# Optimization experiments

Hardware: AMD Instinct MI355X
Metric: run time of the kernel (lower is better)

Reference implementation:

```python
import jax, jax.numpy as jnp
import numpy as np

ALPHA_MAX = 0.1


def setup_inputs() -> dict:
    key = jax.random.key(0)
    ks = jax.random.split(key, 9)
    B, M, L = 256, 3, 100000
    A, H = 4096, 512
    return {
        "x": jax.random.uniform(ks[0], (B, M, L), dtype=jnp.float32),  # log1p scores, non-negative
        "active_idx": jax.random.randint(ks[1], (A,), 0, L, dtype=jnp.int64 if jax.config.jax_enable_x64 else jnp.int32),
        "global_logits": jnp.log(jnp.full((M,), 1.0 / M, dtype=jnp.float32) + 1e-12),
        "delta_w": 0.01 * jax.random.normal(ks[2], (M, L), dtype=jnp.float32),
        "bias": 0.01 * jax.random.normal(ks[3], (L,), dtype=jnp.float32),
        "log_alpha": jnp.float32(-3.0),
        "hidden_w": jax.random.normal(ks[4], (H, M * A), dtype=jnp.float32) * (1.0 / np.sqrt(M * A)),
        "hidden_b": 0.01 * jax.random.normal(ks[5], (H,), dtype=jnp.float32),
        "delta_layer_w": jax.random.normal(ks[6], (A, H), dtype=jnp.float32) * (1.0 / np.sqrt(H)),
        "delta_layer_b": 0.01 * jax.random.normal(ks[7], (A,), dtype=jnp.float32),
    }


def reference(x, active_idx, global_logits, delta_w, bias, log_alpha,
              hidden_w, hidden_b, delta_layer_w, delta_layer_b):
    B = x.shape[0]
    # base logits: elementwise weighted sum over the 3 models, per-label weights
    w_eff = jax.nn.softmax(global_logits)[:, None] + delta_w          # (M, L)
    logits = jnp.einsum("bml,ml->bl", x, w_eff) + bias                # (B, L)
    # gather active labels -> 2-layer MLP (dropout is identity in eval)
    x_active = x[:, :, active_idx].reshape(B, -1)                     # (B, M*A)
    h = jax.nn.relu(x_active @ hidden_w.T + hidden_b)                 # (B, H)
    delta_active = h @ delta_layer_w.T + delta_layer_b                # (B, A)
    # scaled scatter-add back into full logits (duplicates accumulate)
    alpha = ALPHA_MAX * jax.nn.sigmoid(log_alpha)
    logits = logits.at[:, active_idx].add(alpha * delta_active)
    return logits
```

## Files before the change

kernel.cpp:

```cpp
#include <hip/hip_runtime.h>
#include <math.h>

#define B_ 256
#define M_ 3
#define L_ 100000
#define A_ 4096
#define H_ 512
#define MA_ (M_*A_)
#define K1_ MA_
#define NZ_ 16
#define KC1_ (K1_/NZ_)
#define BCHUNK_ 4

typedef __attribute__((ext_vector_type(8))) short bf16x8;
typedef __attribute__((ext_vector_type(8))) unsigned short u16x8;
typedef __attribute__((ext_vector_type(4))) float f32x4;

static __device__ __forceinline__ float4 ld4(const float* p) {
    return *reinterpret_cast<const float4*>(p);
}
static __device__ __forceinline__ void st4(float* p, float4 v) {
    *reinterpret_cast<float4*>(p) = v;
}
static __device__ __forceinline__ unsigned short f2bf(float f) {
    unsigned u = __float_as_uint(f);
    unsigned r = (u + 0x7FFFu + ((u >> 16) & 1u)) >> 16;
    return (unsigned short)r;
}
static __device__ __forceinline__ float getc(const float4& v, int c) {
    switch (c) { case 0: return v.x; case 1: return v.y; case 2: return v.z; default: return v.w; }
}

__global__ void init_head(int* __restrict__ head) {
    int i = blockIdx.x * blockDim.x + threadIdx.x;
    if (i < L_) head[i] = -1;
}

__global__ void build_chain(const int* __restrict__ idx, int* __restrict__ head,
                            int* __restrict__ next) {
    int a = blockIdx.x * blockDim.x + threadIdx.x;
    if (a < A_) next[a] = atomicExch(&head[idx[a]], a);
}

__global__ void f32_to_bf16(const float* __restrict__ in, unsigned short* __restrict__ out, int n8) {
    int i = blockIdx.x * blockDim.x + threadIdx.x;
    if (i >= n8) return;
    float4 v0 = ld4(in + (size_t)i * 8);
    float4 v1 = ld4(in + (size_t)i * 8 + 4);
    u16x8 o;
    o[0] = f2bf(v0.x); o[1] = f2bf(v0.y); o[2] = f2bf(v0.z); o[3] = f2bf(v0.w);
    o[4] = f2bf(v1.x); o[5] = f2bf(v1.y); o[6] = f2bf(v1.z); o[7] = f2bf(v1.w);
    *reinterpret_cast<u16x8*>(out + (size_t)i * 8) = o;
}

__global__ __launch_bounds__(256) void logits_gather(
    const float* __restrict__ x, const float* __restrict__ gl,
    const float* __restrict__ dw, const float* __restrict__ bias,
    const int* __restrict__ head, const int* __restrict__ next,
    float* __restrict__ logits, unsigned short* __restrict__ xa) {
    const int L4 = L_ / 4;
    int i = blockIdx.x * blockDim.x + threadIdx.x;
    if (i >= L4) return;
    int l = i * 4;
    int b0 = blockIdx.y * BCHUNK_;

    float g0 = gl[0], g1 = gl[1], g2 = gl[2];
    float mx = fmaxf(g0, fmaxf(g1, g2));
    float e0 = expf(g0 - mx), e1 = expf(g1 - mx), e2 = expf(g2 - mx);
    float inv = 1.0f / (e0 + e1 + e2);
    float s0 = e0 * inv, s1 = e1 * inv, s2 = e2 * inv;

    float4 d0 = ld4(dw + l);
    float4 d1 = ld4(dw + L_ + l);
    float4 d2 = ld4(dw + 2 * L_ + l);
    float4 bb = ld4(bias + l);
    float4 w0 = make_float4(s0 + d0.x, s0 + d0.y, s0 + d0.z, s0 + d0.w);
    float4 w1 = make_float4(s1 + d1.x, s1 + d1.y, s1 + d1.z, s1 + d1.w);
    float4 w2 = make_float4(s2 + d2.x, s2 + d2.y, s2 + d2.z, s2 + d2.w);

    float4 X[BCHUNK_][3];
    #pragma unroll
    for (int c = 0; c < BCHUNK_; ++c) {
        const float* xb = x + (size_t)(b0 + c) * M_ * L_ + l;
        X[c][0] = ld4(xb);
        X[c][1] = ld4(xb + L_);
        X[c][2] = ld4(xb + 2 * L_);
    }
    #pragma unroll
    for (int c = 0; c < BCHUNK_; ++c) {
        float4 o;
        o.x = X[c][0].x * w0.x + X[c][1].x * w1.x + X[c][2].x * w2.x + bb.x;
        o.y = X[c][0].y * w0.y + X[c][1].y * w1.y + X[c][2].y * w2.y + bb.y;
        o.z = X[c][0].z * w0.z + X[c][1].z * w1.z + X[c][2].z * w2.z + bb.z;
        o.w = X[c][0].w * w0.w + X[c][1].w * w1.w + X[c][2].w * w2.w + bb.w;
        st4(logits + (size_t)(b0 + c) * L_ + l, o);
    }

    #pragma unroll
    for (int c = 0; c < 4; ++c) {
        int a = head[l + c];
        while (a >= 0) {
            #pragma unroll
            for (int b = 0; b < BCHUNK_; ++b) {
                unsigned short* xab = xa + (size_t)(b0 + b) * MA_;
                xab[a]            = f2bf(getc(X[b][0], c));
                xab[A_ + a]       = f2bf(getc(X[b][1], c));
                xab[2 * A_ + a]   = f2bf(getc(X[b][2], c));
            }
            a = next[a];
        }
    }
}

__global__ __launch_bounds__(256) void gemm1_mfma(
    const unsigned short* __restrict__ Xa, const unsigned short* __restrict__ W,
    float* __restrict__ part) {
    int tid = threadIdx.x;
    int wave = tid >> 6, lane = tid & 63;
    int row0 = blockIdx.x * 64 + (wave >> 1) * 32;
    int col0 = blockIdx.y * 64 + (wave & 1) * 32;
    int k0 = blockIdx.z * KC1_;
    int lr = lane & 15;
    int lk = (lane >> 4) * 8;
    const unsigned short* pa0 = Xa + (size_t)(row0 + lr) * K1_ + k0 + lk;
    const unsigned short* pa1 = pa0 + (size_t)16 * K1_;
    const unsigned short* pb0 = W + (size_t)(col0 + lr) * K1_ + k0 + lk;
    const unsigned short* pb1 = pb0 + (size_t)16 * K1_;
    f32x4 acc00 = {0.f,0.f,0.f,0.f}, acc01 = {0.f,0.f,0.f,0.f};
    f32x4 acc10 = {0.f,0.f,0.f,0.f}, acc11 = {0.f,0.f,0.f,0.f};
    #pragma unroll 4
    for (int k = 0; k < KC1_; k += 32) {
        bf16x8 a0 = *reinterpret_cast<const bf16x8*>(pa0 + k);
        bf16x8 a1 = *reinterpret_cast<const bf16x8*>(pa1 + k);
        bf16x8 b0 = *reinterpret_cast<const bf16x8*>(pb0 + k);
        bf16x8 b1 = *reinterpret_cast<const bf16x8*>(pb1 + k);
        acc00 = __builtin_amdgcn_mfma_f32_16x16x32_bf16(a0, b0, acc00, 0, 0, 0);
        acc01 = __builtin_amdgcn_mfma_f32_16x16x32_bf16(a0, b1, acc01, 0, 0, 0);
        acc10 = __builtin_amdgcn_mfma_f32_16x16x32_bf16(a1, b0, acc10, 0, 0, 0);
        acc11 = __builtin_amdgcn_mfma_f32_16x16x32_bf16(a1, b1, acc11, 0, 0, 0);
    }
    float* base = part + (size_t)blockIdx.z * B_ * H_;
    #pragma unroll
    for (int j = 0; j < 4; ++j) {
        int r = (lane >> 4) * 4 + j;
        base[(size_t)(row0 + r) * H_ + col0 + lr]           = acc00[j];
        base[(size_t)(row0 + r) * H_ + col0 + 16 + lr]      = acc01[j];
        base[(size_t)(row0 + 16 + r) * H_ + col0 + lr]      = acc10[j];
        base[(size_t)(row0 + 16 + r) * H_ + col0 + 16 + lr] = acc11[j];
    }
}

__global__ void reduce_relu(const float* __restrict__ part,
                            const float* __restrict__ hb,
                            unsigned short* __restrict__ h) {
    int t = blockIdx.x * blockDim.x + threadIdx.x;
    if (t >= B_ * H_) return;
    int n = t & (H_ - 1);
    float s = hb[n];
    #pragma unroll
    for (int z = 0; z < NZ_; ++z) s += part[(size_t)z * B_ * H_ + t];
    h[t] = f2bf(fmaxf(s, 0.0f));
}

__global__ __launch_bounds__(256) void gemm2_mfma(
    const unsigned short* __restrict__ Hm, const unsigned short* __restrict__ W2,
    const float* __restrict__ b2, const float* __restrict__ la,
    float* __restrict__ da) {
    int tid = threadIdx.x;
    int wave = tid >> 6, lane = tid & 63;
    int row0 = blockIdx.x * 64 + (wave >> 1) * 32;
    int col0 = blockIdx.y * 64 + (wave & 1) * 32;
    int lr = lane & 15;
    int lk = (lane >> 4) * 8;
    const unsigned short* pa0 = Hm + (size_t)(row0 + lr) * H_ + lk;
    const unsigned short* pa1 = pa0 + (size_t)16 * H_;
    const unsigned short* pb0 = W2 + (size_t)(col0 + lr) * H_ + lk;
    const unsigned short* pb1 = pb0 + (size_t)16 * H_;
    f32x4 acc00 = {0.f,0.f,0.f,0.f}, acc01 = {0.f,0.f,0.f,0.f};
    f32x4 acc10 = {0.f,0.f,0.f,0.f}, acc11 = {0.f,0.f,0.f,0.f};
    #pragma unroll 4
    for (int k = 0; k < H_; k += 32) {
        bf16x8 a0 = *reinterpret_cast<const bf16x8*>(pa0 + k);
        bf16x8 a1 = *reinterpret_cast<const bf16x8*>(pa1 + k);
        bf16x8 b0 = *reinterpret_cast<const bf16x8*>(pb0 + k);
        bf16x8 b1 = *reinterpret_cast<const bf16x8*>(pb1 + k);
        acc00 = __builtin_amdgcn_mfma_f32_16x16x32_bf16(a0, b0, acc00, 0, 0, 0);
        acc01 = __builtin_amdgcn_mfma_f32_16x16x32_bf16(a0, b1, acc01, 0, 0, 0);
        acc10 = __builtin_amdgcn_mfma_f32_16x16x32_bf16(a1, b0, acc10, 0, 0, 0);
        acc11 = __builtin_amdgcn_mfma_f32_16x16x32_bf16(a1, b1, acc11, 0, 0, 0);
    }
    float alpha = 0.1f / (1.0f + expf(-la[0]));
    #pragma unroll
    for (int j = 0; j < 4; ++j) {
        int r = (lane >> 4) * 4 + j;
        int c0 = col0 + lr, c1 = col0 + 16 + lr;
        da[(size_t)(row0 + r) * A_ + c0]      = alpha * (acc00[j] + b2[c0]);
        da[(size_t)(row0 + r) * A_ + c1]      = alpha * (acc01[j] + b2[c1]);
        da[(size_t)(row0 + 16 + r) * A_ + c0] = alpha * (acc10[j] + b2[c0]);
        da[(size_t)(row0 + 16 + r) * A_ + c1] = alpha * (acc11[j] + b2[c1]);
    }
}

__global__ void scatter_add(const float* __restrict__ da, const int* __restrict__ idx,
                            const int* __restrict__ head, const int* __restrict__ next,
                            float* __restrict__ logits) {
    int t = blockIdx.x * blockDim.x + threadIdx.x;
    if (t >= B_ * A_) return;
    int a = t & (A_ - 1);
    int b = t >> 12;
    int l = idx[a];
    if (head[l] != a) return;
    float s = 0.0f;
    for (int aa = a; aa >= 0; aa = next[aa]) s += da[(size_t)b * A_ + aa];
    logits[(size_t)b * L_ + l] += s;
}

static inline size_t align256(size_t x) { return (x + 255) & ~(size_t)255; }

extern "C" void kernel_launch(void* const* d_in, const int* in_sizes, int n_in,
                              void* d_out, int out_size, void* d_ws, size_t ws_size,
                              hipStream_t stream) {
    const float* x    = (const float*)d_in[0];
    const int*   idx  = (const int*)d_in[1];
    const float* gl   = (const float*)d_in[2];
    const float* dw   = (const float*)d_in[3];
    const float* bias = (const float*)d_in[4];
    const float* la   = (const float*)d_in[5];
    const float* hw   = (const float*)d_in[6];
    const float* hb   = (const float*)d_in[7];
    const float* w2   = (const float*)d_in[8];
    const float* b2   = (const float*)d_in[9];
    float* logits = (float*)d_out;

    char* ws = (char*)d_ws;
    int* head = (int*)ws;              ws += align256((size_t)L_ * 4);
    int* next = (int*)ws;              ws += align256((size_t)A_ * 4);
    unsigned short* xa = (unsigned short*)ws;   ws += align256((size_t)B_ * MA_ * 2);
    unsigned short* hwb = (unsigned short*)ws;  ws += align256((size_t)H_ * MA_ * 2);
    unsigned short* w2b = (unsigned short*)ws;  ws += align256((size_t)A_ * H_ * 2);
    float* part = (float*)ws;          ws += align256((size_t)NZ_ * B_ * H_ * 4);
    unsigned short* h = (unsigned short*)ws;    ws += align256((size_t)B_ * H_ * 2);
    float* da = part;

    init_head<<<(L_ + 255) / 256, 256, 0, stream>>>(head);
    build_chain<<<(A_ + 255) / 256, 256, 0, stream>>>(idx, head, next);

    f32_to_bf16<<<(H_ * MA_ / 8 + 255) / 256, 256, 0, stream>>>(hw, hwb, H_ * MA_ / 8);
    f32_to_bf16<<<(A_ * H_ / 8 + 255) / 256, 256, 0, stream>>>(w2, w2b, A_ * H_ / 8);

    dim3 g1((L_ / 4 + 255) / 256, B_ / BCHUNK_);
    logits_gather<<<g1, 256, 0, stream>>>(x, gl, dw, bias, head, next, logits, xa);

    gemm1_mfma<<<dim3(B_ / 64, H_ / 64, NZ_), 256, 0, stream>>>(xa, hwb, part);
    reduce_relu<<<(B_ * H_ + 255) / 256, 256, 0, stream>>>(part, hb, h);
    gemm2_mfma<<<dim3(B_ / 64, A_ / 64), 256, 0, stream>>>(h, w2b, b2, la, da);
    scatter_add<<<(B_ * A_ + 255) / 256, 256, 0, stream>>>(da, idx, head, next, logits);
}
```

Measured before the change: 202.7 us.

## Fuse weight bf16 conversion into GEMMs and scatter-add into gemm2 epilogue

Drops the separate f32-to-bf16 conversion kernels for both weight matrices and converts fp32 weights to bf16 inside the MFMA loops instead. The scatter_add kernel and its intermediate delta buffer are removed, and gemm2 atomically adds its scaled outputs straight into logits at idx positions. The gather kernel now handles 8 labels per thread with vectorized head loads. Together these cut launches and intermediate traffic. In exchange the GEMMs read twice the weight bytes and spend ALU on conversion, and the random atomics make duplicate-index accumulation order nondeterministic.

Measured after the change: 257.9 us. 27.2% more time.

```diff
diff --git a/kernel.cpp b/kernel.cpp
--- a/kernel.cpp
+++ b/kernel.cpp
@@ -13,7 +13,6 @@
 #define BCHUNK_ 4
 
 typedef __attribute__((ext_vector_type(8))) short bf16x8;
-typedef __attribute__((ext_vector_type(8))) unsigned short u16x8;
 typedef __attribute__((ext_vector_type(4))) float f32x4;
 
 static __device__ __forceinline__ float4 ld4(const float* p) {
@@ -27,30 +26,27 @@
     unsigned r = (u + 0x7FFFu + ((u >> 16) & 1u)) >> 16;
     return (unsigned short)r;
 }
+static __device__ __forceinline__ bf16x8 cvt8(float4 a, float4 b) {
+    bf16x8 o;
+    o[0] = (short)f2bf(a.x); o[1] = (short)f2bf(a.y);
+    o[2] = (short)f2bf(a.z); o[3] = (short)f2bf(a.w);
+    o[4] = (short)f2bf(b.x); o[5] = (short)f2bf(b.y);
+    o[6] = (short)f2bf(b.z); o[7] = (short)f2bf(b.w);
+    return o;
+}
 static __device__ __forceinline__ float getc(const float4& v, int c) {
     switch (c) { case 0: return v.x; case 1: return v.y; case 2: return v.z; default: return v.w; }
 }
 
 __global__ void init_head(int* __restrict__ head) {
     int i = blockIdx.x * blockDim.x + threadIdx.x;
-    if (i < L_) head[i] = -1;
+    if (i < L_ / 4) *reinterpret_cast<int4*>(head + i * 4) = make_int4(-1, -1, -1, -1);
 }
 
 __global__ void build_chain(const int* __restrict__ idx, int* __restrict__ head,
                             int* __restrict__ next) {
     int a = blockIdx.x * blockDim.x + threadIdx.x;
     if (a < A_) next[a] = atomicExch(&head[idx[a]], a);
-}
-
-__global__ void f32_to_bf16(const float* __restrict__ in, unsigned short* __restrict__ out, int n8) {
-    int i = blockIdx.x * blockDim.x + threadIdx.x;
-    if (i >= n8) return;
-    float4 v0 = ld4(in + (size_t)i * 8);
-    float4 v1 = ld4(in + (size_t)i * 8 + 4);
-    u16x8 o;
-    o[0] = f2bf(v0.x); o[1] = f2bf(v0.y); o[2] = f2bf(v0.z); o[3] = f2bf(v0.w);
-    o[4] = f2bf(v1.x); o[5] = f2bf(v1.y); o[6] = f2bf(v1.z); o[7] = f2bf(v1.w);
-    *reinterpret_cast<u16x8*>(out + (size_t)i * 8) = o;
 }
 
 __global__ __launch_bounds__(256) void logits_gather(
@@ -58,54 +54,67 @@
     const float* __restrict__ dw, const float* __restrict__ bias,
     const int* __restrict__ head, const int* __restrict__ next,
     float* __restrict__ logits, unsigned short* __restrict__ xa) {
-    const int L4 = L_ / 4;
+    const int L8 = L_ / 8;
     int i = blockIdx.x * blockDim.x + threadIdx.x;
-    if (i >= L4) return;
-    int l = i * 4;
+    if (i >= L8) return;
+    int l = i * 8;
     int b0 = blockIdx.y * BCHUNK_;
 
     float g0 = gl[0], g1 = gl[1], g2 = gl[2];
     float mx = fmaxf(g0, fmaxf(g1, g2));
     float e0 = expf(g0 - mx), e1 = expf(g1 - mx), e2 = expf(g2 - mx);
     float inv = 1.0f / (e0 + e1 + e2);
-    float s0 = e0 * inv, s1 = e1 * inv, s2 = e2 * inv;
-
-    float4 d0 = ld4(dw + l);
-    float4 d1 = ld4(dw + L_ + l);
-    float4 d2 = ld4(dw + 2 * L_ + l);
-    float4 bb = ld4(bias + l);
-    float4 w0 = make_float4(s0 + d0.x, s0 + d0.y, s0 + d0.z, s0 + d0.w);
-    float4 w1 = make_float4(s1 + d1.x, s1 + d1.y, s1 + d1.z, s1 + d1.w);
-    float4 w2 = make_float4(s2 + d2.x, s2 + d2.y, s2 + d2.z, s2 + d2.w);
-
-    float4 X[BCHUNK_][3];
+    float sm[3] = {e0 * inv, e1 * inv, e2 * inv};
+
+    float4 w[3][2], bb[2];
+    #pragma unroll
+    for (int m = 0; m < 3; ++m) {
+        float4 dA = ld4(dw + (size_t)m * L_ + l);
+        float4 dB = ld4(dw + (size_t)m * L_ + l + 4);
+        w[m][0] = make_float4(sm[m] + dA.x, sm[m] + dA.y, sm[m] + dA.z, sm[m] + dA.w);
+        w[m][1] = make_float4(sm[m] + dB.x, sm[m] + dB.y, sm[m] + dB.z, sm[m] + dB.w);
+    }
+    bb[0] = ld4(bias + l);
+    bb[1] = ld4(bias + l + 4);
+
+    int heads[8];
+    *reinterpret_cast<int4*>(heads) = *reinterpret_cast<const int4*>(head + l);
+    *reinterpret_cast<int4*>(heads + 4) = *reinterpret_cast<const int4*>(head + l + 4);
+
+    float4 X[BCHUNK_][3][2];
     #pragma unroll
     for (int c = 0; c < BCHUNK_; ++c) {
         const float* xb = x + (size_t)(b0 + c) * M_ * L_ + l;
-        X[c][0] = ld4(xb);
-        X[c][1] = ld4(xb + L_);
-        X[c][2] = ld4(xb + 2 * L_);
+        #pragma unroll
+        for (int m = 0; m < 3; ++m) {
+            X[c][m][0] = ld4(xb + (size_t)m * L_);
+            X[c][m][1] = ld4(xb + (size_t)m * L_ + 4);
+        }
     }
     #pragma unroll
     for (int c = 0; c < BCHUNK_; ++c) {
-        float4 o;
-        o.x = X[c][0].x * w0.x + X[c][1].x * w1.x + X[c][2].x * w2.x + bb.x;
-        o.y = X[c][0].y * w0.y + X[c][1].y * w1.y + X[c][2].y * w2.y + bb.y;
-        o.z = X[c][0].z * w0.z + X[c][1].z * w1.z + X[c][2].z * w2.z + bb.z;
-        o.w = X[c][0].w * w0.w + X[c][1].w * w1.w + X[c][2].w * w2.w + bb.w;
-        st4(logits + (size_t)(b0 + c) * L_ + l, o);
-    }
-
-    #pragma unroll
-    for (int c = 0; c < 4; ++c) {
-        int a = head[l + c];
+        #pragma unroll
+        for (int hh = 0; hh < 2; ++hh) {
+            float4 o;
+            o.x = X[c][0][hh].x * w[0][hh].x + X[c][1][hh].x * w[1][hh].x + X[c][2][hh].x * w[2][hh].x + bb[hh].x;
+            o.y = X[c][0][hh].y * w[0][hh].y + X[c][1][hh].y * w[1][hh].y + X[c][2][hh].y * w[2][hh].y + bb[hh].y;
+            o.z = X[c][0][hh].z * w[0][hh].z + X[c][1][hh].z * w[1][hh].z + X[c][2][hh].z * w[2][hh].z + bb[hh].z;
+            o.w = X[c][0][hh].w * w[0][hh].w + X[c][1][hh].w * w[1][hh].w + X[c][2][hh].w * w[2][hh].w + bb[hh].w;
+            st4(logits + (size_t)(b0 + c) * L_ + l + hh * 4, o);
+        }
+    }
+
+    #pragma unroll
+    for (int p = 0; p < 8; ++p) {
+        int a = heads[p];
+        int hh = p >> 2, c = p & 3;
         while (a >= 0) {
             #pragma unroll
             for (int b = 0; b < BCHUNK_; ++b) {
                 unsigned short* xab = xa + (size_t)(b0 + b) * MA_;
-                xab[a]            = f2bf(getc(X[b][0], c));
-                xab[A_ + a]       = f2bf(getc(X[b][1], c));
-                xab[2 * A_ + a]   = f2bf(getc(X[b][2], c));
+                xab[a]          = f2bf(getc(X[b][0][hh], c));
+                xab[A_ + a]     = f2bf(getc(X[b][1][hh], c));
+                xab[2 * A_ + a] = f2bf(getc(X[b][2][hh], c));
             }
             a = next[a];
         }
@@ -113,7 +122,7 @@
 }
 
 __global__ __launch_bounds__(256) void gemm1_mfma(
-    const unsigned short* __restrict__ Xa, const unsigned short* __restrict__ W,
+    const unsigned short* __restrict__ Xa, const float* __restrict__ W,
     float* __restrict__ part) {
     int tid = threadIdx.x;
     int wave = tid >> 6, lane = tid & 63;
@@ -124,16 +133,16 @@
     int lk = (lane >> 4) * 8;
     const unsigned short* pa0 = Xa + (size_t)(row0 + lr) * K1_ + k0 + lk;
     const unsigned short* pa1 = pa0 + (size_t)16 * K1_;
-    const unsigned short* pb0 = W + (size_t)(col0 + lr) * K1_ + k0 + lk;
-    const unsigned short* pb1 = pb0 + (size_t)16 * K1_;
+    const float* pb0 = W + (size_t)(col0 + lr) * K1_ + k0 + lk;
+    const float* pb1 = pb0 + (size_t)16 * K1_;
     f32x4 acc00 = {0.f,0.f,0.f,0.f}, acc01 = {0.f,0.f,0.f,0.f};
     f32x4 acc10 = {0.f,0.f,0.f,0.f}, acc11 = {0.f,0.f,0.f,0.f};
     #pragma unroll 4
     for (int k = 0; k < KC1_; k += 32) {
         bf16x8 a0 = *reinterpret_cast<const bf16x8*>(pa0 + k);
         bf16x8 a1 = *reinterpret_cast<const bf16x8*>(pa1 + k);
-        bf16x8 b0 = *reinterpret_cast<const bf16x8*>(pb0 + k);
-        bf16x8 b1 = *reinterpret_cast<const bf16x8*>(pb1 + k);
+        bf16x8 b0 = cvt8(ld4(pb0 + k), ld4(pb0 + k + 4));
+        bf16x8 b1 = cvt8(ld4(pb1 + k), ld4(pb1 + k + 4));
         acc00 = __builtin_amdgcn_mfma_f32_16x16x32_bf16(a0, b0, acc00, 0, 0, 0);
         acc01 = __builtin_amdgcn_mfma_f32_16x16x32_bf16(a0, b1, acc01, 0, 0, 0);
         acc10 = __builtin_amdgcn_mfma_f32_16x16x32_bf16(a1, b0, acc10, 0, 0, 0);
@@ -162,10 +171,10 @@
     h[t] = f2bf(fmaxf(s, 0.0f));
 }
 
-__global__ __launch_bounds__(256) void gemm2_mfma(
-    const unsigned short* __restrict__ Hm, const unsigned short* __restrict__ W2,
+__global__ __launch_bounds__(256) void gemm2_scatter(
+    const unsigned short* __restrict__ Hm, const float* __restrict__ W2,
     const float* __restrict__ b2, const float* __restrict__ la,
-    float* __restrict__ da) {
+    const int* __restrict__ idx, float* __restrict__ logits) {
     int tid = threadIdx.x;
     int wave = tid >> 6, lane = tid & 63;
     int row0 = blockIdx.x * 64 + (wave >> 1) * 32;
@@ -174,45 +183,33 @@
     int lk = (lane >> 4) * 8;
     const unsigned short* pa0 = Hm + (size_t)(row0 + lr) * H_ + lk;
     const unsigned short* pa1 = pa0 + (size_t)16 * H_;
-    const unsigned short* pb0 = W2 + (size_t)(col0 + lr) * H_ + lk;
-    const unsigned short* pb1 = pb0 + (size_t)16 * H_;
+    const float* pb0 = W2 + (size_t)(col0 + lr) * H_ + lk;
+    const float* pb1 = pb0 + (size_t)16 * H_;
     f32x4 acc00 = {0.f,0.f,0.f,0.f}, acc01 = {0.f,0.f,0.f,0.f};
     f32x4 acc10 = {0.f,0.f,0.f,0.f}, acc11 = {0.f,0.f,0.f,0.f};
     #pragma unroll 4
     for (int k = 0; k < H_; k += 32) {
         bf16x8 a0 = *reinterpret_cast<const bf16x8*>(pa0 + k);
         bf16x8 a1 = *reinterpret_cast<const bf16x8*>(pa1 + k);
-        bf16x8 b0 = *reinterpret_cast<const bf16x8*>(pb0 + k);
-        bf16x8 b1 = *reinterpret_cast<const bf16x8*>(pb1 + k);
+        bf16x8 b0 = cvt8(ld4(pb0 + k), ld4(pb0 + k + 4));
+        bf16x8 b1 = cvt8(ld4(pb1 + k), ld4(pb1 + k + 4));
         acc00 = __builtin_amdgcn_mfma_f32_16x16x32_bf16(a0, b0, acc00, 0, 0, 0);
         acc01 = __builtin_amdgcn_mfma_f32_16x16x32_bf16(a0, b1, acc01, 0, 0, 0);
         acc10 = __builtin_amdgcn_mfma_f32_16x16x32_bf16(a1, b0, acc10, 0, 0, 0);
         acc11 = __builtin_amdgcn_mfma_f32_16x16x32_bf16(a1, b1, acc11, 0, 0, 0);
     }
     float alpha = 0.1f / (1.0f + expf(-la[0]));
+    int c0 = col0 + lr, c1 = col0 + 16 + lr;
+    int l0 = idx[c0], l1 = idx[c1];
+    float bias0 = b2[c0], bias1 = b2[c1];
     #pragma unroll
     for (int j = 0; j < 4; ++j) {
         int r = (lane >> 4) * 4 + j;
-        int c0 = col0 + lr, c1 = col0 + 16 + lr;
-        da[(size_t)(row0 + r) * A_ + c0]      = alpha * (acc00[j] + b2[c0]);
-        da[(size_t)(row0 + r) * A_ + c1]      = alpha * (acc01[j] + b2[c1]);
-        da[(size_t)(row0 + 16 + r) * A_ + c0] = alpha * (acc10[j] + b2[c0]);
-        da[(size_t)(row0 + 16 + r) * A_ + c1] = alpha * (acc11[j] + b2[c1]);
-    }
-}
-
-__global__ void scatter_add(const float* __restrict__ da, const int* __restrict__ idx,
-                            const int* __restrict__ head, const int* __restrict__ next,
-                            float* __restrict__ logits) {
-    int t = blockIdx.x * blockDim.x + threadIdx.x;
-    if (t >= B_ * A_) return;
-    int a = t & (A_ - 1);
-    int b = t >> 12;
-    int l = idx[a];
-    if (head[l] != a) return;
-    float s = 0.0f;
-    for (int aa = a; aa >= 0; aa = next[aa]) s += da[(size_t)b * A_ + aa];
-    logits[(size_t)b * L_ + l] += s;
+        atomicAdd(&logits[(size_t)(row0 + r) * L_ + l0],      alpha * (acc00[j] + bias0));
+        atomicAdd(&logits[(size_t)(row0 + r) * L_ + l1],      alpha * (acc01[j] + bias1));
+        atomicAdd(&logits[(size_t)(row0 + 16 + r) * L_ + l0], alpha * (acc10[j] + bias0));
+        atomicAdd(&logits[(size_t)(row0 + 16 + r) * L_ + l1], alpha * (acc11[j] + bias1));
+    }
 }
 
 static inline size_t align256(size_t x) { return (x + 255) & ~(size_t)255; }
@@ -233,26 +230,19 @@
     float* logits = (float*)d_out;
 
     char* ws = (char*)d_ws;
-    int* head = (int*)ws;              ws += align256((size_t)L_ * 4);
-    int* next = (int*)ws;              ws += align256((size_t)A_ * 4);
-    unsigned short* xa = (unsigned short*)ws;   ws += align256((size_t)B_ * MA_ * 2);
-    unsigned short* hwb = (unsigned short*)ws;  ws += align256((size_t)H_ * MA_ * 2);
-    unsigned short* w2b = (unsigned short*)ws;  ws += align256((size_t)A_ * H_ * 2);
-    float* part = (float*)ws;          ws += align256((size_t)NZ_ * B_ * H_ * 4);
-    unsigned short* h = (unsigned short*)ws;    ws += align256((size_t)B_ * H_ * 2);
-    float* da = part;
-
-    init_head<<<(L_ + 255) / 256, 256, 0, stream>>>(head);
+    int* head = (int*)ws;                      ws += align256((size_t)L_ * 4);
+    int* next = (int*)ws;                      ws += align256((size_t)A_ * 4);
+    unsigned short* xa = (unsigned short*)ws;  ws += align256((size_t)B_ * MA_ * 2);
+    float* part = (float*)ws;                  ws += align256((size_t)NZ_ * B_ * H_ * 4);
+    unsigned short* h = (unsigned short*)ws;   ws += align256((size_t)B_ * H_ * 2);
+
+    init_head<<<(L_ / 4 + 255) / 256, 256, 0, stream>>>(head);
     build_chain<<<(A_ + 255) / 256, 256, 0, stream>>>(idx, head, next);
 
-    f32_to_bf16<<<(H_ * MA_ / 8 + 255) / 256, 256, 0, stream>>>(hw, hwb, H_ * MA_ / 8);
-    f32_to_bf16<<<(A_ * H_ / 8 + 255) / 256, 256, 0, stream>>>(w2, w2b, A_ * H_ / 8);
-
-    dim3 g1((L_ / 4 + 255) / 256, B_ / BCHUNK_);
+    dim3 g1((L_ / 8 + 255) / 256, B_ / BCHUNK_);
     logits_gather<<<g1, 256, 0, stream>>>(x, gl, dw, bias, head, next, logits, xa);
 
-    gemm1_mfma<<<dim3(B_ / 64, H_ / 64, NZ_), 256, 0, stream>>>(xa, hwb, part);
+    gemm1_mfma<<<dim3(B_ / 64, H_ / 64, NZ_), 256, 0, stream>>>(xa, hw, part);
     reduce_relu<<<(B_ * H_ + 255) / 256, 256, 0, stream>>>(part, hb, h);
-    gemm2_mfma<<<dim3(B_ / 64, A_ / 64), 256, 0, stream>>>(h, w2b, b2, la, da);
-    scatter_add<<<(B_ * A_ + 255) / 256, 256, 0, stream>>>(da, idx, head, next, logits);
-}
+    gemm2_scatter<<<dim3(B_ / 64, A_ / 64), 256, 0, stream>>>(h, w2, b2, la, idx, logits);
+}
```

## Fuse second GEMM with atomic scatter-add and convert W2 to bf16 inline

Applied to the files above, without the earlier changes.

Removes the separate W2 f32-to-bf16 conversion kernel and the scatter_add kernel. gemm2 now loads fp32 W2, converts it to bf16 in registers, and atomically adds alpha-scaled outputs directly into logits at idx positions, so duplicate indices are resolved by atomics instead of the chain walk. It also vectorizes init_head and the head loads in the gather kernel. This saves two launches and the da round trip through memory, but adds scattered fp32 atomics and a nondeterministic summation order.

After: 210.6 us. +3.9%, slower.

```diff
diff --git a/kernel.cpp b/kernel.cpp
--- a/kernel.cpp
+++ b/kernel.cpp
@@ -27,13 +27,21 @@
     unsigned r = (u + 0x7FFFu + ((u >> 16) & 1u)) >> 16;
     return (unsigned short)r;
 }
+static __device__ __forceinline__ bf16x8 cvt8(float4 a, float4 b) {
+    bf16x8 o;
+    o[0] = (short)f2bf(a.x); o[1] = (short)f2bf(a.y);
+    o[2] = (short)f2bf(a.z); o[3] = (short)f2bf(a.w);
+    o[4] = (short)f2bf(b.x); o[5] = (short)f2bf(b.y);
+    o[6] = (short)f2bf(b.z); o[7] = (short)f2bf(b.w);
+    return o;
+}
 static __device__ __forceinline__ float getc(const float4& v, int c) {
     switch (c) { case 0: return v.x; case 1: return v.y; case 2: return v.z; default: return v.w; }
 }
 
 __global__ void init_head(int* __restrict__ head) {
     int i = blockIdx.x * blockDim.x + threadIdx.x;
-    if (i < L_) head[i] = -1;
+    if (i < L_ / 4) *reinterpret_cast<int4*>(head + i * 4) = make_int4(-1, -1, -1, -1);
 }
 
 __global__ void build_chain(const int* __restrict__ idx, int* __restrict__ head,
@@ -78,6 +86,8 @@
     float4 w1 = make_float4(s1 + d1.x, s1 + d1.y, s1 + d1.z, s1 + d1.w);
     float4 w2 = make_float4(s2 + d2.x, s2 + d2.y, s2 + d2.z, s2 + d2.w);
 
+    int4 heads = *reinterpret_cast<const int4*>(head + l);
+
     float4 X[BCHUNK_][3];
     #pragma unroll
     for (int c = 0; c < BCHUNK_; ++c) {
@@ -96,16 +106,17 @@
         st4(logits + (size_t)(b0 + c) * L_ + l, o);
     }
 
+    int hs[4] = {heads.x, heads.y, heads.z, heads.w};
     #pragma unroll
     for (int c = 0; c < 4; ++c) {
-        int a = head[l + c];
+        int a = hs[c];
         while (a >= 0) {
             #pragma unroll
             for (int b = 0; b < BCHUNK_; ++b) {
                 unsigned short* xab = xa + (size_t)(b0 + b) * MA_;
-                xab[a]            = f2bf(getc(X[b][0], c));
-                xab[A_ + a]       = f2bf(getc(X[b][1], c));
-                xab[2 * A_ + a]   = f2bf(getc(X[b][2], c));
+                xab[a]          = f2bf(getc(X[b][0], c));
+                xab[A_ + a]     = f2bf(getc(X[b][1], c));
+                xab[2 * A_ + a] = f2bf(getc(X[b][2], c));
             }
             a = next[a];
         }
@@ -162,10 +173,10 @@
     h[t] = f2bf(fmaxf(s, 0.0f));
 }
 
-__global__ __launch_bounds__(256) void gemm2_mfma(
-    const unsigned short* __restrict__ Hm, const unsigned short* __restrict__ W2,
+__global__ __launch_bounds__(256) void gemm2_scatter(
+    const unsigned short* __restrict__ Hm, const float* __restrict__ W2,
     const float* __restrict__ b2, const float* __restrict__ la,
-    float* __restrict__ da) {
+    const int* __restrict__ idx, float* __restrict__ logits) {
     int tid = threadIdx.x;
     int wave = tid >> 6, lane = tid & 63;
     int row0 = blockIdx.x * 64 + (wave >> 1) * 32;
@@ -174,45 +185,33 @@
     int lk = (lane >> 4) * 8;
     const unsigned short* pa0 = Hm + (size_t)(row0 + lr) * H_ + lk;
     const unsigned short* pa1 = pa0 + (size_t)16 * H_;
-    const unsigned short* pb0 = W2 + (size_t)(col0 + lr) * H_ + lk;
-    const unsigned short* pb1 = pb0 + (size_t)16 * H_;
+    const float* pb0 = W2 + (size_t)(col0 + lr) * H_ + lk;
+    const float* pb1 = pb0 + (size_t)16 * H_;
     f32x4 acc00 = {0.f,0.f,0.f,0.f}, acc01 = {0.f,0.f,0.f,0.f};
     f32x4 acc10 = {0.f,0.f,0.f,0.f}, acc11 = {0.f,0.f,0.f,0.f};
     #pragma unroll 4
     for (int k = 0; k < H_; k += 32) {
         bf16x8 a0 = *reinterpret_cast<const bf16x8*>(pa0 + k);
         bf16x8 a1 = *reinterpret_cast<const bf16x8*>(pa1 + k);
-        bf16x8 b0 = *reinterpret_cast<const bf16x8*>(pb0 + k);
-        bf16x8 b1 = *reinterpret_cast<const bf16x8*>(pb1 + k);
+        bf16x8 b0 = cvt8(ld4(pb0 + k), ld4(pb0 + k + 4));
+        bf16x8 b1 = cvt8(ld4(pb1 + k), ld4(pb1 + k + 4));
         acc00 = __builtin_amdgcn_mfma_f32_16x16x32_bf16(a0, b0, acc00, 0, 0, 0);
         acc01 = __builtin_amdgcn_mfma_f32_16x16x32_bf16(a0, b1, acc01, 0, 0, 0);
         acc10 = __builtin_amdgcn_mfma_f32_16x16x32_bf16(a1, b0, acc10, 0, 0, 0);
         acc11 = __builtin_amdgcn_mfma_f32_16x16x32_bf16(a1, b1, acc11, 0, 0, 0);
     }
     float alpha = 0.1f / (1.0f + expf(-la[0]));
+    int c0 = col0 + lr, c1 = col0 + 16 + lr;
+    int l0 = idx[c0], l1 = idx[c1];
+    float bias0 = b2[c0], bias1 = b2[c1];
     #pragma unroll
     for (int j = 0; j < 4; ++j) {
         int r = (lane >> 4) * 4 + j;
-        int c0 = col0 + lr, c1 = col0 + 16 + lr;
-        da[(size_t)(row0 + r) * A_ + c0]      = alpha * (acc00[j] + b2[c0]);
-        da[(size_t)(row0 + r) * A_ + c1]      = alpha * (acc01[j] + b2[c1]);
-        da[(size_t)(row0 + 16 + r) * A_ + c0] = alpha * (acc10[j] + b2[c0]);
-        da[(size_t)(row0 + 16 + r) * A_ + c1] = alpha * (acc11[j] + b2[c1]);
-    }
-}
-
-__global__ void scatter_add(const float* __restrict__ da, const int* __restrict__ idx,
-                            const int* __restrict__ head, const int* __restrict__ next,
-                            float* __restrict__ logits) {
-    int t = blockIdx.x * blockDim.x + threadIdx.x;
-    if (t >= B_ * A_) return;
-    int a = t & (A_ - 1);
-    int b = t >> 12;
-    int l = idx[a];
-    if (head[l] != a) return;
-    float s = 0.0f;
-    for (int aa = a; aa >= 0; aa = next[aa]) s += da[(size_t)b * A_ + aa];
-    logits[(size_t)b * L_ + l] += s;
+        atomicAdd(&logits[(size_t)(row0 + r) * L_ + l0],      alpha * (acc00[j] + bias0));
+        atomicAdd(&logits[(size_t)(row0 + r) * L_ + l1],      alpha * (acc01[j] + bias1));
+        atomicAdd(&logits[(size_t)(row0 + 16 + r) * L_ + l0], alpha * (acc10[j] + bias0));
+        atomicAdd(&logits[(size_t)(row0 + 16 + r) * L_ + l1], alpha * (acc11[j] + bias1));
+    }
 }
 
 static inline size_t align256(size_t x) { return (x + 255) & ~(size_t)255; }
@@ -233,26 +232,22 @@
     float* logits = (float*)d_out;
 
     char* ws = (char*)d_ws;
-    int* head = (int*)ws;              ws += align256((size_t)L_ * 4);
-    int* next = (int*)ws;              ws += align256((size_t)A_ * 4);
-    unsigned short* xa = (unsigned short*)ws;   ws += align256((size_t)B_ * MA_ * 2);
-    unsigned short* hwb = (unsigned short*)ws;  ws += align256((size_t)H_ * MA_ * 2);
-    unsigned short* w2b = (unsigned short*)ws;  ws += align256((size_t)A_ * H_ * 2);
-    float* part = (float*)ws;          ws += align256((size_t)NZ_ * B_ * H_ * 4);
-    unsigned short* h = (unsigned short*)ws;    ws += align256((size_t)B_ * H_ * 2);
-    float* da = part;
-
-    init_head<<<(L_ + 255) / 256, 256, 0, stream>>>(head);
+    int* head = (int*)ws;                      ws += align256((size_t)L_ * 4);
+    int* next = (int*)ws;                      ws += align256((size_t)A_ * 4);
+    unsigned short* xa = (unsigned short*)ws;  ws += align256((size_t)B_ * MA_ * 2);
+    unsigned short* hwb = (unsigned short*)ws; ws += align256((size_t)H_ * MA_ * 2);
+    float* part = (float*)ws;                  ws += align256((size_t)NZ_ * B_ * H_ * 4);
+    unsigned short* h = (unsigned short*)ws;   ws += align256((size_t)B_ * H_ * 2);
+
+    init_head<<<(L_ / 4 + 255) / 256, 256, 0, stream>>>(head);
     build_chain<<<(A_ + 255) / 256, 256, 0, stream>>>(idx, head, next);
 
     f32_to_bf16<<<(H_ * MA_ / 8 + 255) / 256, 256, 0, stream>>>(hw, hwb, H_ * MA_ / 8);
-    f32_to_bf16<<<(A_ * H_ / 8 + 255) / 256, 256, 0, stream>>>(w2, w2b, A_ * H_ / 8);
 
     dim3 g1((L_ / 4 + 255) / 256, B_ / BCHUNK_);
     logits_gather<<<g1, 256, 0, stream>>>(x, gl, dw, bias, head, next, logits, xa);
 
     gemm1_mfma<<<dim3(B_ / 64, H_ / 64, NZ_), 256, 0, stream>>>(xa, hwb, part);
     reduce_relu<<<(B_ * H_ + 255) / 256, 256, 0, stream>>>(part, hb, h);
-    gemm2_mfma<<<dim3(B_ / 64, A_ / 64), 256, 0, stream>>>(h, w2b, b2, la, da);
-    scatter_add<<<(B_ * A_ + 255) / 256, 256, 0, stream>>>(da, idx, head, next, logits);
-}
+    gemm2_scatter<<<dim3(B_ / 64, A_ / 64), 256, 0, stream>>>(h, w2, b2, la, idx, logits);
+}
```
